# Kernel optimization log

Hardware: AMD Instinct MI355X
Metric: run time of the kernel (lower is better)

Reference implementation:

```python
import math
import jax, jax.numpy as jnp
import numpy as np

B, D, T, C, H = 4096, 1024, 768, 16, 4
CURV = 0.05
EPS = 1e-8
ASINH_MAX = float(np.arcsinh(2.0 ** 15))

# ---------- Poincare ball ops (hyptorch.pmath) ----------

def artanh(x):
    x = jnp.clip(x, -1 + 1e-5, 1 - 1e-5)
    return 0.5 * (jnp.log1p(x) - jnp.log1p(-x))

def p_logmap0(y, c):
    sc = c ** 0.5
    n = jnp.clip(jnp.linalg.norm(y, axis=-1, keepdims=True), 1e-15, None)
    return y / (n * sc) * artanh(sc * n)

def p_expmap0(u, c):
    sc = c ** 0.5
    n = jnp.clip(jnp.linalg.norm(u, axis=-1, keepdims=True), 1e-15, None)
    return jnp.tanh(sc * n) * u / (sc * n)

def p_project(x, c):
    maxn = (1 - 4e-3) / c ** 0.5  # float32 eps in hyptorch
    n = jnp.clip(jnp.linalg.norm(x, axis=-1, keepdims=True), 1e-15, None)
    return jnp.where(n > maxn, x / n * maxn, x)

# ---------- Lorentz ops (MERU-style L module) ----------

def l_expmap0(x, c):
    rc = (c ** 0.5) * jnp.linalg.norm(x, axis=-1, keepdims=True)
    si = jnp.clip(rc, EPS, ASINH_MAX)
    return jnp.sinh(si) * x / jnp.clip(rc, EPS, None)

def l_logmap0(x, c):
    rc = (c ** 0.5) * jnp.linalg.norm(x, axis=-1, keepdims=True)
    return jnp.arcsinh(rc) * x / jnp.clip(rc, EPS, None)

def oxy_angle(x, y, c):
    xt = jnp.sqrt(1.0 / c + jnp.sum(x * x, -1))
    yt = jnp.sqrt(1.0 / c + jnp.sum(y * y, -1))
    c_xyl = c * (jnp.sum(x * y, -1) - xt * yt)
    num = yt + c_xyl * xt
    den = jnp.sqrt(jnp.clip(c_xyl ** 2 - 1.0, EPS, None))
    acos_in = num / (jnp.linalg.norm(x, axis=-1) * den + EPS)
    return jnp.arccos(jnp.clip(acos_in, -1 + EPS, 1 - EPS))

def half_aperture(x, c, min_radius=0.1):
    asin_in = 2.0 * min_radius / (jnp.linalg.norm(x, axis=-1) * c ** 0.5 + EPS)
    return jnp.arcsin(jnp.clip(asin_in, -1 + EPS, 1 - EPS))

# ---------- small building blocks ----------

def layernorm(x, w, b, eps=1e-5):
    mu = jnp.mean(x, -1, keepdims=True)
    var = jnp.mean((x - mu) ** 2, -1, keepdims=True)
    return (x - mu) * jax.lax.rsqrt(var + eps) * w + b

def mha(x, w_in, b_in, w_out, b_out):
    # x: (B, S=4, D), torch nn.MultiheadAttention, batch_first, 4 heads
    Bq, S, Dm = x.shape
    hd = Dm // H
    qkv = x @ w_in.T + b_in
    q, k, v = jnp.split(qkv, 3, axis=-1)
    rs = lambda t: t.reshape(Bq, S, H, hd).transpose(0, 2, 1, 3)
    q, k, v = rs(q), rs(k), rs(v)
    a = jax.nn.softmax(jnp.einsum('bhqd,bhkd->bhqk', q, k) / math.sqrt(hd), axis=-1)
    o = jnp.einsum('bhqk,bhkd->bhqd', a, v).transpose(0, 2, 1, 3).reshape(Bq, S, Dm)
    return o @ w_out.T + b_out

def mobius_add_batch(x, y, c):
    # x: (C, D) (the -p points), y: (B, D) -> (C, B, D)
    xy = x @ y.T                               # (C, B)
    x2 = jnp.sum(x * x, -1, keepdims=True)     # (C, 1)
    y2 = jnp.sum(y * y, -1)                    # (B,)
    num = (1 + 2 * c * xy + c * y2[None, :])[..., None] * x[:, None, :] \
        + (1 - c * x2)[..., None] * y[None, :, :]
    den = 1 + 2 * c * xy + c * c * x2 * y2[None, :]
    return num / (den[..., None] + 1e-5)

def hyperbolic_mlr(x, a, p, c):
    sc = c ** 0.5
    p_p = p_expmap0(p, c)                      # (C, D)
    conf = 1 - c * jnp.sum(p_p ** 2, -1, keepdims=True)
    a_p = a * conf                             # (C, D)
    lam = 2.0 / (1 - c * jnp.sum(p_p ** 2, -1))
    a_norm = jnp.linalg.norm(a_p, axis=-1)     # (C,)
    kk = lam * a_norm / sc
    mob = mobius_add_batch(-p_p, x, c)         # (C, B, D)
    num = 2 * sc * jnp.einsum('cbd,cd->cb', mob, a_p)
    den = a_norm[:, None] * (1 - c * jnp.sum(mob ** 2, -1))
    return (kk[:, None] * jnp.arcsinh(num / den)).T  # (B, C)

def hyp_loss_fn(order_hyp, family_hyp, order, family, mask,
                to_w, to_b, tf_w, tf_b):
    order_feats = l_expmap0(order @ to_w.T + to_b, CURV)
    order_loss = jnp.mean(jax.nn.relu(
        oxy_angle(order_feats, family_hyp, CURV) - half_aperture(order_feats, CURV)))
    fam_feats = l_expmap0(family @ tf_w.T + tf_b, CURV)
    fpen = jax.nn.relu(
        oxy_angle(fam_feats, order_hyp, CURV) - half_aperture(fam_feats, CURV))
    m = mask.astype(order.dtype)
    cnt = jnp.sum(m)
    family_loss = jnp.where(cnt > 0, jnp.sum(fpen * m) / jnp.clip(cnt, 1.0, None), 0.0)
    return order_loss + family_loss


def setup_inputs() -> dict:
    key = jax.random.key(0)
    ks = jax.random.split(key, 20)
    g = lambda k, s, sc: jax.random.normal(k, s, jnp.float32) * sc
    inp = {
        # Poincare-ball points: scale down so sqrt(c)*||x|| << 1
        'order_hyp': g(ks[0], (B, D), 0.02),
        'family_hyp': g(ks[1], (B, D), 0.02),
        'order_euc': g(ks[2], (B, D), 1.0),
        'family_euc': g(ks[3], (B, D), 1.0),
        'order': g(ks[4], (B, T), 1.0),
        'family': g(ks[5], (B, T), 1.0),
        'mask': jax.random.randint(ks[6], (B,), 0, 2, jnp.int32),
        # MultiheadAttention params
        'in_proj_w': g(ks[7], (3 * D, D), D ** -0.5),
        'in_proj_b': jnp.zeros((3 * D,), jnp.float32),
        'out_proj_w': g(ks[8], (D, D), D ** -0.5),
        'out_proj_b': jnp.zeros((D,), jnp.float32),
        # LayerNorm
        'ln_w': jnp.ones((D,), jnp.float32),
        'ln_b': jnp.zeros((D,), jnp.float32),
        # text projections
        'to_w': g(ks[9], (D, T), T ** -0.5),
        'to_b': jnp.zeros((D,), jnp.float32),
        'tf_w': g(ks[10], (D, T), T ** -0.5),
        'tf_b': jnp.zeros((D,), jnp.float32),
        # HyperbolicMLR params
        'mlr_a': g(ks[11], (C, D), 0.02),
        'mlr_p': g(ks[12], (C, D), 0.02),
    }
    return inp


def reference(order_hyp, family_hyp, order_euc, family_euc, order, family, mask,
              in_proj_w, in_proj_b, out_proj_w, out_proj_b, ln_w, ln_b,
              to_w, to_b, tf_w, tf_b, mlr_a, mlr_p):
    # FromPoincare (logmap0 on the ball)
    fh_e = p_logmap0(family_hyp, CURV)
    oh_e = p_logmap0(order_hyp, CURV)
    gf = jnp.stack([oh_e, fh_e, order_euc, family_euc], axis=1)  # (B, 4, D)
    attn = mha(gf, in_proj_w, in_proj_b, out_proj_w, out_proj_b)
    gf = layernorm(gf + attn, ln_w, ln_b)
    oh, fh, oeu, feu = gf[:, 0], gf[:, 1], gf[:, 2], gf[:, 3]
    fh = l_expmap0(fh, CURV)
    oh = l_expmap0(oh, CURV)
    hyp_loss = hyp_loss_fn(oh, fh, order, family, mask, to_w, to_b, tf_w, tf_b)
    oh_out = l_logmap0(oh, CURV)
    hyp_pt = p_project(p_expmap0(oh_out, CURV), CURV)  # ToPoincare(riemannian=False)
    logits = hyperbolic_mlr(hyp_pt, mlr_a, mlr_p, CURV)
    return (logits, hyp_loss, oh, fh, oeu, feu)
```

## Files before the change

kernel.cpp:

```cpp
#include <hip/hip_runtime.h>
#include <stdint.h>

#define BB    4096
#define DD    1024
#define TT    768
#define CC    16
#define HH    4
#define SS    4
#define HD    256
#define M1    (BB*SS)
#define CURVF 0.05f
#define SCF   0.22360679774997896f
#define EPSF  1e-8f
#define ASINH_MAXF 11.090354888959125f

#define OFF_LOGITS 0ull
#define OFF_LOSS   65536ull
#define OFF_OH     65537ull
#define OFF_FH     (65537ull + 4194304ull)
#define OFF_OEU    (65537ull + 2ull*4194304ull)
#define OFF_FEU    (65537ull + 3ull*4194304ull)

typedef __attribute__((ext_vector_type(8))) short bf16x8;
typedef __attribute__((ext_vector_type(4))) float f32x4;

__device__ __forceinline__ float bf2f(unsigned short h) {
  union { unsigned int u; float f; } v; v.u = ((unsigned int)h) << 16; return v.f;
}
__device__ __forceinline__ unsigned short f2bf(float f) {
  union { float f; unsigned int u; } v; v.f = f;
  unsigned int u = v.u;
  return (unsigned short)((u + 0x7FFFu + ((u >> 16) & 1u)) >> 16);
}
__device__ __forceinline__ ushort4 f2bf4(float4 v) {
  ushort4 o; o.x = f2bf(v.x); o.y = f2bf(v.y); o.z = f2bf(v.z); o.w = f2bf(v.w);
  return o;
}
__device__ __forceinline__ float wsum(float v) {
#pragma unroll
  for (int o = 32; o > 0; o >>= 1) v += __shfl_xor(v, o, 64);
  return v;
}
__device__ __forceinline__ float block_sum(float v, float* red) {
  v = wsum(v);
  int lane = threadIdx.x & 63, wv = threadIdx.x >> 6;
  __syncthreads();
  if (lane == 0) red[wv] = v;
  __syncthreads();
  return red[0] + red[1] + red[2] + red[3];
}
__device__ __forceinline__ float artanh_clip(float x) {
  x = fminf(fmaxf(x, -1.0f + 1e-5f), 1.0f - 1e-5f);
  return 0.5f * (log1pf(x) - log1pf(-x));
}

typedef __attribute__((address_space(1))) const void gas_void;
typedef __attribute__((address_space(3))) void las_void;
__device__ __forceinline__ void gld16(void* l, const void* g) {
  __builtin_amdgcn_global_load_lds((gas_void*)g, (las_void*)l, 16, 0, 0);
}

#define VMCNT(n) asm volatile("s_waitcnt vmcnt(" #n ")" ::: "memory")

struct Cvt6 {
  const float4* src[6];
  unsigned short* dst[6];
  unsigned int end4[6];
};

__device__ __forceinline__ void prep_gf_body(const float* __restrict__ ohyp,
    const float* __restrict__ fhyp, const float* __restrict__ oeuc,
    const float* __restrict__ feuc, unsigned short* __restrict__ gf,
    int b, float* red) {
  int t = threadIdx.x;
  size_t base4 = (size_t)b * (DD / 4);
  float4 xo = ((const float4*)ohyp)[base4 + t];
  float4 xf = ((const float4*)fhyp)[base4 + t];
  float so = xo.x * xo.x + xo.y * xo.y + xo.z * xo.z + xo.w * xo.w;
  float sf = xf.x * xf.x + xf.y * xf.y + xf.z * xf.z + xf.w * xf.w;
  float no2 = block_sum(so, red);
  float nf2 = block_sum(sf, red);
  float no = fmaxf(sqrtf(no2), 1e-15f);
  float nf = fmaxf(sqrtf(nf2), 1e-15f);
  float fo = artanh_clip(SCF * no) / (no * SCF);
  float ff = artanh_clip(SCF * nf) / (nf * SCF);
  size_t g0 = (size_t)b * 4 * (DD / 4);
  float4 e2 = ((const float4*)oeuc)[base4 + t];
  float4 e3 = ((const float4*)feuc)[base4 + t];
  float4 y0 = {xo.x * fo, xo.y * fo, xo.z * fo, xo.w * fo};
  float4 y1 = {xf.x * ff, xf.y * ff, xf.z * ff, xf.w * ff};
  ((ushort4*)gf)[g0 + t]              = f2bf4(y0);
  ((ushort4*)gf)[g0 + DD / 4 + t]     = f2bf4(y1);
  ((ushort4*)gf)[g0 + 2 * DD / 4 + t] = f2bf4(e2);
  ((ushort4*)gf)[g0 + 3 * DD / 4 + t] = f2bf4(e3);
}

__device__ __forceinline__ void mlr_prep_body(const float* __restrict__ a,
    const float* __restrict__ p, float* __restrict__ p_p, float* __restrict__ a_p,
    float* __restrict__ cs, int c, float* red) {
  int t = threadIdx.x;
  size_t base4 = (size_t)c * (DD / 4);
  float4 pv = ((const float4*)p)[base4 + t];
  float4 av = ((const float4*)a)[base4 + t];
  float sp = pv.x * pv.x + pv.y * pv.y + pv.z * pv.z + pv.w * pv.w;
  float sa = av.x * av.x + av.y * av.y + av.z * av.z + av.w * av.w;
  float spa = pv.x * av.x + pv.y * av.y + pv.z * av.z + pv.w * av.w;
  sp = block_sum(sp, red); sa = block_sum(sa, red); spa = block_sum(spa, red);
  float n = fmaxf(sqrtf(sp), 1e-15f);
  float f = tanhf(SCF * n) / (SCF * n);
  float x2 = f * f * sp;
  float conf = 1.0f - CURVF * x2;
  float a_norm = fabsf(conf) * sqrtf(sa);
  float lam = 2.0f / (1.0f - CURVF * x2);
  float kk = lam * a_norm / SCF;
  float xa = -f * conf * spa;
  float4 pp = {pv.x * f, pv.y * f, pv.z * f, pv.w * f};
  float4 ap = {av.x * conf, av.y * conf, av.z * conf, av.w * conf};
  ((float4*)p_p)[base4 + t] = pp;
  ((float4*)a_p)[base4 + t] = ap;
  if (threadIdx.x == 0) {
    cs[c * 5 + 0] = x2; cs[c * 5 + 1] = conf; cs[c * 5 + 2] = a_norm;
    cs[c * 5 + 3] = kk; cs[c * 5 + 4] = xa;
  }
}

__global__ __launch_bounds__(256) void k_front(
    const float* __restrict__ ohyp, const float* __restrict__ fhyp,
    const float* __restrict__ oeuc, const float* __restrict__ feuc,
    unsigned short* __restrict__ gf,
    const float* __restrict__ mlr_a, const float* __restrict__ mlr_p,
    float* __restrict__ p_p, float* __restrict__ a_p, float* __restrict__ cs,
    Cvt6 cv, unsigned int total4) {
  __shared__ float red[4];
  unsigned int blk = blockIdx.x;
  if (blk < BB) {
    prep_gf_body(ohyp, fhyp, oeuc, feuc, gf, (int)blk, red);
    return;
  }
  if (blk < BB + CC) {
    mlr_prep_body(mlr_a, mlr_p, p_p, a_p, cs, (int)(blk - BB), red);
    return;
  }
  unsigned int i = (blk - BB - CC) * 256 + threadIdx.x;
  if (i >= total4) return;
#pragma unroll
  for (int j = 0; j < 6; j++) {
    if (i < cv.end4[j]) {
      unsigned int k = i - (j ? cv.end4[j - 1] : 0u);
      ((ushort4*)cv.dst[j])[k] = f2bf4(cv.src[j][k]);
      return;
    }
  }
}

template <int OUT_BF16>
__global__ __launch_bounds__(512) void k_gemm256(
    const unsigned short* __restrict__ A, const unsigned short* __restrict__ Bm,
    const float* __restrict__ bias, void* __restrict__ Cv,
    int N, int K, int nx) {
  __shared__ unsigned short lds[4][2][8192];
  const int nwg = gridDim.x;
  const int rid = blockIdx.x;
  const int wg = (rid & 7) * (nwg >> 3) + (rid >> 3);
  const int bx = wg % nx;
  const int by = wg / nx;
  const long tileM = (long)by * 256;
  const long tileN = (long)bx * 256;
  const int tid = threadIdx.x;
  const int lane = tid & 63;
  const int wv = tid >> 6;
  const int wr = wv >> 2;
  const int wc = wv & 3;
  const int NT = K >> 5;

  f32x4 acc[8][4];
#pragma unroll
  for (int i = 0; i < 8; i++)
#pragma unroll
    for (int j = 0; j < 4; j++) acc[i][j] = (f32x4){0.f, 0.f, 0.f, 0.f};

  const int srow = tid >> 2;
  const int lc = (tid & 3) ^ ((srow >> 1) & 3);
  const unsigned short* Ag = A + (tileM + srow) * (long)K + lc * 8;
  const unsigned short* Bg = Bm + (tileN + srow) * (long)K + lc * 8;

  auto stageA = [&](int t) {
    int b = t & 3;
    const unsigned short* s = Ag + t * 32;
    gld16(&lds[b][0][tid * 8], s);
    gld16(&lds[b][0][4096 + tid * 8], s + (long)128 * K);
  };
  auto stageB = [&](int t) {
    int b = t & 3;
    const unsigned short* s = Bg + t * 32;
    gld16(&lds[b][1][tid * 8], s);
    gld16(&lds[b][1][4096 + tid * 8], s + (long)128 * K);
  };

  stageA(0); stageB(0);
  stageA(1); stageB(1);
  stageA(2); stageB(2);
  VMCNT(8);
  __builtin_amdgcn_s_barrier();
  asm volatile("" ::: "memory");

  const int fr = lane & 15;
  const int hi = lane >> 4;
  const int fko = (hi ^ ((fr >> 1) & 3)) * 8;

  for (int t = 0; t < NT; ++t) {
    const unsigned short* Ab = &lds[t & 3][0][0];
    const unsigned short* Bb = &lds[t & 3][1][0];
    bf16x8 af[4], bfr[4];
#pragma unroll
    for (int j = 0; j < 4; j++)
      bfr[j] = *(const bf16x8*)(Bb + (wc * 64 + j * 16 + fr) * 32 + fko);
#pragma unroll
    for (int i = 0; i < 4; i++)
      af[i] = *(const bf16x8*)(Ab + (wr * 128 + i * 16 + fr) * 32 + fko);
    if (t + 3 < NT) stageA(t + 3);
    __builtin_amdgcn_s_setprio(1);
#pragma unroll
    for (int i = 0; i < 4; i++)
#pragma unroll
      for (int j = 0; j < 4; j++)
        acc[i][j] = __builtin_amdgcn_mfma_f32_16x16x32_bf16(af[i], bfr[j], acc[i][j], 0, 0, 0);
    __builtin_amdgcn_s_setprio(0);
#pragma unroll
    for (int i = 0; i < 4; i++)
      af[i] = *(const bf16x8*)(Ab + (wr * 128 + (i + 4) * 16 + fr) * 32 + fko);
    if (t + 3 < NT) stageB(t + 3);
    __builtin_amdgcn_s_setprio(1);
#pragma unroll
    for (int i = 0; i < 4; i++)
#pragma unroll
      for (int j = 0; j < 4; j++)
        acc[i + 4][j] = __builtin_amdgcn_mfma_f32_16x16x32_bf16(af[i], bfr[j], acc[i + 4][j], 0, 0, 0);
    __builtin_amdgcn_s_setprio(0);
    if (t + 1 < NT) {
      if (t + 3 < NT)      VMCNT(8);
      else if (t + 2 < NT) VMCNT(4);
      else                 VMCNT(0);
      __builtin_amdgcn_s_barrier();
      asm volatile("" ::: "memory");
    }
  }

  const int er = hi * 4;
#pragma unroll
  for (int i = 0; i < 8; i++) {
#pragma unroll
    for (int j = 0; j < 4; j++) {
      long col = tileN + wc * 64 + j * 16 + fr;
      float bv = bias ? bias[col] : 0.f;
#pragma unroll
      for (int r = 0; r < 4; r++) {
        long row = tileM + wr * 128 + i * 16 + er + r;
        float v = acc[i][j][r] + bv;
        if (OUT_BF16) ((unsigned short*)Cv)[row * (long)N + col] = f2bf(v);
        else          ((float*)Cv)[row * (long)N + col] = v;
      }
    }
  }
}

template <int OUT_BF16>
__device__ __forceinline__ void gemm_body(
    unsigned short* As, unsigned short* Bs,
    const unsigned short* __restrict__ A, const unsigned short* __restrict__ Bm,
    const float* __restrict__ bias, void* __restrict__ Cv,
    int M, int N, int K, int bx, int by) {
  const int tid = threadIdx.x;
  const int lane = tid & 63;
  const int wv = tid >> 6;
  const long tileM = (long)by * 128;
  const long tileN = (long)bx * 128;

  f32x4 acc[4][4];
#pragma unroll
  for (int i = 0; i < 4; i++)
#pragma unroll
    for (int j = 0; j < 4; j++) acc[i][j] = (f32x4){0.f, 0.f, 0.f, 0.f};

  const int srow = wv * 16 + (lane >> 2);
  const int lc = (lane & 3) ^ ((srow >> 1) & 3);
  const unsigned short* Ag = A + (tileM + srow) * (long)K + lc * 8;
  const unsigned short* Bg = Bm + (tileN + srow) * (long)K + lc * 8;
  unsigned short* Asl = As + srow * 32 + (lane & 3) * 8;
  unsigned short* Bsl = Bs + srow * 32 + (lane & 3) * 8;

  const int fr = lane & 15;
  const int rkey = (fr >> 1) & 3;
  const int fko2 = (((lane >> 4) ^ rkey)) * 8;
  const int wr = (wv >> 1) * 64;
  const int wc = (wv & 1) * 64;

  for (int k0 = 0; k0 < K; k0 += 32) {
    gld16(Asl, Ag + k0);
    gld16(Asl + 64 * 32, Ag + (long)64 * K + k0);
    gld16(Bsl, Bg + k0);
    gld16(Bsl + 64 * 32, Bg + (long)64 * K + k0);
    __syncthreads();
    bf16x8 af[4], bfr[4];
#pragma unroll
    for (int i = 0; i < 4; i++)
      af[i] = *(const bf16x8*)(As + (wr + i * 16 + fr) * 32 + fko2);
#pragma unroll
    for (int j = 0; j < 4; j++)
      bfr[j] = *(const bf16x8*)(Bs + (wc + j * 16 + fr) * 32 + fko2);
#pragma unroll
    for (int i = 0; i < 4; i++)
#pragma unroll
      for (int j = 0; j < 4; j++)
        acc[i][j] = __builtin_amdgcn_mfma_f32_16x16x32_bf16(af[i], bfr[j], acc[i][j], 0, 0, 0);
    __syncthreads();
  }

  const int er = (lane >> 4) * 4;
  const int ec = lane & 15;
#pragma unroll
  for (int i = 0; i < 4; i++) {
#pragma unroll
    for (int j = 0; j < 4; j++) {
      long col = tileN + wc + j * 16 + ec;
      float bv = bias ? bias[col] : 0.f;
#pragma unroll
      for (int r = 0; r < 4; r++) {
        long row = tileM + wr + i * 16 + er + r;
        float v = acc[i][j][r] + bv;
        if (OUT_BF16) ((unsigned short*)Cv)[row * (long)N + col] = f2bf(v);
        else          ((float*)Cv)[row * (long)N + col] = v;
      }
    }
  }
}

__global__ __launch_bounds__(256) void k_gemm_loss(
    const unsigned short* __restrict__ A0, const unsigned short* __restrict__ B0,
    const float* __restrict__ b0, float* __restrict__ C0,
    const unsigned short* __restrict__ A1, const unsigned short* __restrict__ B1,
    const float* __restrict__ b1, float* __restrict__ C1, int M, int N, int K) {
  __shared__ unsigned short As[128 * 32];
  __shared__ unsigned short Bs[128 * 32];
  if (blockIdx.z == 0)
    gemm_body<0>(As, Bs, A0, B0, b0, C0, M, N, K, blockIdx.x, blockIdx.y);
  else
    gemm_body<0>(As, Bs, A1, B1, b1, C1, M, N, K, blockIdx.x, blockIdx.y);
}

__global__ __launch_bounds__(256) void k_attn(const unsigned short* __restrict__ qkv,
                                              unsigned short* __restrict__ o) {
  int b = blockIdx.x;
  int h = blockIdx.y;
  int lane = threadIdx.x & 63;
  int qi = threadIdx.x >> 6;
  const unsigned short* base = qkv + (size_t)b * 4 * 3072 + h * HD;
  int d = lane * 4;
  float qv[4], kv[4][4], vv[4][4];
  {
    ushort4 q4 = *(const ushort4*)(base + (size_t)qi * 3072 + d);
    qv[0] = bf2f(q4.x); qv[1] = bf2f(q4.y); qv[2] = bf2f(q4.z); qv[3] = bf2f(q4.w);
  }
#pragma unroll
  for (int j = 0; j < 4; j++) {
    ushort4 k4 = *(const ushort4*)(base + (size_t)j * 3072 + 1024 + d);
    ushort4 v4 = *(const ushort4*)(base + (size_t)j * 3072 + 2048 + d);
    kv[j][0] = bf2f(k4.x); kv[j][1] = bf2f(k4.y); kv[j][2] = bf2f(k4.z); kv[j][3] = bf2f(k4.w);
    vv[j][0] = bf2f(v4.x); vv[j][1] = bf2f(v4.y); vv[j][2] = bf2f(v4.z); vv[j][3] = bf2f(v4.w);
  }
  float sc_[4];
#pragma unroll
  for (int j = 0; j < 4; j++) {
    float p = 0.f;
#pragma unroll
    for (int t = 0; t < 4; t++) p += qv[t] * kv[j][t];
    sc_[j] = wsum(p) * (1.0f / 16.0f);
  }
  float mx = fmaxf(fmaxf(sc_[0], sc_[1]), fmaxf(sc_[2], sc_[3]));
  float e[4], den = 0.f;
#pragma unroll
  for (int j = 0; j < 4; j++) { e[j] = expf(sc_[j] - mx); den += e[j]; }
  float inv = 1.0f / den;
  float4 ov = {0.f, 0.f, 0.f, 0.f};
#pragma unroll
  for (int j = 0; j < 4; j++) {
    float w = e[j] * inv;
    ov.x += w * vv[j][0]; ov.y += w * vv[j][1];
    ov.z += w * vv[j][2]; ov.w += w * vv[j][3];
  }
  *(ushort4*)(o + (size_t)(b * 4 + qi) * DD + h * HD + d) = f2bf4(ov);
}

__global__ __launch_bounds__(256) void k_ln_split(const unsigned short* __restrict__ gf,
    const unsigned short* __restrict__ attn, const float* __restrict__ lnw,
    const float* __restrict__ lnb, float* __restrict__ dout) {
  __shared__ float red[4];
  int r = blockIdx.x;
  int b = r >> 2, s = r & 3;
  int t = threadIdx.x;
  size_t base4 = (size_t)r * (DD / 4);
  ushort4 g4 = ((const ushort4*)gf)[base4 + t];
  ushort4 a4 = ((const ushort4*)attn)[base4 + t];
  float x[4] = {bf2f(g4.x) + bf2f(a4.x), bf2f(g4.y) + bf2f(a4.y),
                bf2f(g4.z) + bf2f(a4.z), bf2f(g4.w) + bf2f(a4.w)};
  float sum = x[0] + x[1] + x[2] + x[3];
  float sq = x[0] * x[0] + x[1] * x[1] + x[2] * x[2] + x[3] * x[3];
  sum = block_sum(sum, red);
  sq  = block_sum(sq, red);
  float mu = sum * (1.0f / (float)DD);
  float var = sq * (1.0f / (float)DD) - mu * mu;
  float inv = rsqrtf(var + 1e-5f);
  float4 w4 = ((const float4*)lnw)[t];
  float4 b4 = ((const float4*)lnb)[t];
  float y[4];
  y[0] = (x[0] - mu) * inv * w4.x + b4.x;
  y[1] = (x[1] - mu) * inv * w4.y + b4.y;
  y[2] = (x[2] - mu) * inv * w4.z + b4.z;
  y[3] = (x[3] - mu) * inv * w4.w + b4.w;
  float fmul = 1.0f;
  if (s < 2) {
    float n2 = y[0] * y[0] + y[1] * y[1] + y[2] * y[2] + y[3] * y[3];
    n2 = block_sum(n2, red);
    float rc = SCF * sqrtf(n2);
    float si = fminf(fmaxf(rc, EPSF), ASINH_MAXF);
    fmul = sinhf(si) / fmaxf(rc, EPSF);
  }
  size_t offs = (s == 0) ? OFF_OH : (s == 1) ? OFF_FH : (s == 2) ? OFF_OEU : OFF_FEU;
  float4* outp = (float4*)(dout + offs + (size_t)b * DD);
  float4 o4 = {y[0] * fmul, y[1] * fmul, y[2] * fmul, y[3] * fmul};
  outp[t] = o4;
}

__global__ __launch_bounds__(256) void k_oxy(const float* __restrict__ raw0,
    const float* __restrict__ y0, const float* __restrict__ raw1,
    const float* __restrict__ y1, float* __restrict__ pens) {
  __shared__ float red[4];
  int b = blockIdx.x;
  int which = blockIdx.y;
  const float* raw = which ? raw1 : raw0;
  const float* yr  = which ? y1 : y0;
  size_t base = (size_t)b * DD;
  float sxx = 0.f, sxy = 0.f, syy = 0.f;
#pragma unroll
  for (int k = 0; k < 4; k++) {
    int d = threadIdx.x + 256 * k;
    float xv = raw[base + d];
    float yv = yr[base + d];
    sxx += xv * xv; sxy += xv * yv; syy += yv * yv;
  }
  sxx = block_sum(sxx, red);
  sxy = block_sum(sxy, red);
  syy = block_sum(syy, red);
  if (threadIdx.x == 0) {
    float nraw = sqrtf(sxx);
    float rc = SCF * nraw;
    float si = fminf(fmaxf(rc, EPSF), ASINH_MAXF);
    float f = sinhf(si) / fmaxf(rc, EPSF);
    float x2 = f * f * sxx;
    float xy = f * sxy;
    float y2 = syy;
    float nx = f * nraw;
    float xt = sqrtf(1.0f / CURVF + x2);
    float yt = sqrtf(1.0f / CURVF + y2);
    float c_xyl = CURVF * (xy - xt * yt);
    float num = yt + c_xyl * xt;
    float den = sqrtf(fmaxf(c_xyl * c_xyl - 1.0f, EPSF));
    float ai = num / (nx * den + EPSF);
    ai = fminf(fmaxf(ai, -1.0f + EPSF), 1.0f - EPSF);
    float ang = acosf(ai);
    float asi = 0.2f / (nx * SCF + EPSF);
    asi = fminf(fmaxf(asi, -1.0f + EPSF), 1.0f - EPSF);
    float ap = asinf(asi);
    pens[(size_t)which * BB + b] = fmaxf(ang - ap, 0.0f);
  }
}

__global__ __launch_bounds__(256) void k_back(const float* __restrict__ oh,
    const float* __restrict__ p_p, const float* __restrict__ a_p,
    const float* __restrict__ cs, float* __restrict__ logits,
    const float* __restrict__ pens, const int* __restrict__ mask,
    float* __restrict__ dout) {
  __shared__ float row[DD];
  __shared__ float dots[CC][2];
  __shared__ float s_n2;
  __shared__ float red[4];
  int blk = blockIdx.x;
  int lane = threadIdx.x & 63, wv = threadIdx.x >> 6;

  if (blk == BB) {
    float s0 = 0.f, s1 = 0.f, cnt = 0.f;
    for (int i = threadIdx.x; i < BB; i += 256) {
      s0 += pens[i];
      float m = (float)mask[i];
      s1 += pens[BB + i] * m;
      cnt += m;
    }
    s0 = block_sum(s0, red);
    s1 = block_sum(s1, red);
    cnt = block_sum(cnt, red);
    if (threadIdx.x == 0) {
      float order_loss = s0 / (float)BB;
      float fam = (cnt > 0.f) ? s1 / fmaxf(cnt, 1.0f) : 0.0f;
      dout[OFF_LOSS] = order_loss + fam;
    }
    return;
  }

  int b = blk;
  const float* src = oh + (size_t)b * DD;
#pragma unroll
  for (int k = 0; k < 4; k++)
    row[threadIdx.x + 256 * k] = src[threadIdx.x + 256 * k];
  __syncthreads();
  if (wv == 0) {
    float n2p = 0.f;
#pragma unroll
    for (int k = 0; k < 4; k++) {
      float4 v = ((const float4*)row)[lane + 64 * k];
      n2p += v.x * v.x + v.y * v.y + v.z * v.z + v.w * v.w;
    }
    n2p = wsum(n2p);
    if (lane == 0) s_n2 = n2p;
  }
#pragma unroll
  for (int ccc = 0; ccc < 4; ccc++) {
    int c = wv * 4 + ccc;
    const float4* pp4 = (const float4*)(p_p + (size_t)c * DD);
    const float4* ap4 = (const float4*)(a_p + (size_t)c * DD);
    float dp = 0.f, da = 0.f;
#pragma unroll
    for (int k = 0; k < 4; k++) {
      int d4 = lane + 64 * k;
      float4 v = ((const float4*)row)[d4];
      float4 p4 = pp4[d4];
      float4 a4 = ap4[d4];
      dp += p4.x * v.x + p4.y * v.y + p4.z * v.z + p4.w * v.w;
      da += a4.x * v.x + a4.y * v.y + a4.z * v.z + a4.w * v.w;
    }
    dp = wsum(dp); da = wsum(da);
    if (lane == 0) { dots[c][0] = dp; dots[c][1] = da; }
  }
  __syncthreads();
  if (threadIdx.x < CC) {
    int c = threadIdx.x;
    float n2 = s_n2;
    float n1 = sqrtf(n2);
    float rc = SCF * n1;
    float g = asinhf(rc) / fmaxf(rc, EPSF);
    float nu = fmaxf(n1 * g, 1e-15f);
    float fac = tanhf(SCF * nu) / (SCF * nu);
    float s = g * fac;
    float ny = fmaxf(n1 * s, 1e-15f);
    float maxn = (1.0f - 0.004f) / SCF;
    if (ny > maxn) s *= maxn / ny;
    float y2 = s * s * n2;
    float py = s * dots[c][0];
    float ay = s * dots[c][1];
    float x2 = cs[c * 5 + 0], conf = cs[c * 5 + 1], a_norm = cs[c * 5 + 2];
    float kk = cs[c * 5 + 3], xa = cs[c * 5 + 4];
    float xy = -py;
    float A = 1.f + 2.f * CURVF * xy + CURVF * y2;
    float den0 = 1.f + 2.f * CURVF * xy + CURVF * CURVF * x2 * y2;
    float d = den0 + 1e-5f;
    float num = 2.f * SCF * (A * xa + conf * ay) / d;
    float mob2 = (A * A * x2 + 2.f * A * conf * xy + conf * conf * y2) / (d * d);
    float denl = a_norm * (1.f - CURVF * mob2);
    logits[(size_t)b * CC + c] = kk * asinhf(num / denl);
  }
}

extern "C" void kernel_launch(void* const* d_in, const int* in_sizes, int n_in,
                              void* d_out, int out_size, void* d_ws, size_t ws_size,
                              hipStream_t stream) {
  const float* order_hyp  = (const float*)d_in[0];
  const float* family_hyp = (const float*)d_in[1];
  const float* order_euc  = (const float*)d_in[2];
  const float* family_euc = (const float*)d_in[3];
  const float* order      = (const float*)d_in[4];
  const float* family     = (const float*)d_in[5];
  const int*   mask       = (const int*)d_in[6];
  const float* in_proj_w  = (const float*)d_in[7];
  const float* in_proj_b  = (const float*)d_in[8];
  const float* out_proj_w = (const float*)d_in[9];
  const float* out_proj_b = (const float*)d_in[10];
  const float* ln_w       = (const float*)d_in[11];
  const float* ln_b       = (const float*)d_in[12];
  const float* to_w       = (const float*)d_in[13];
  const float* to_b       = (const float*)d_in[14];
  const float* tf_w       = (const float*)d_in[15];
  const float* tf_b       = (const float*)d_in[16];
  const float* mlr_a      = (const float*)d_in[17];
  const float* mlr_p      = (const float*)d_in[18];
  float* dout = (float*)d_out;

  char* w = (char*)d_ws;
  size_t off = 0;
  auto take = [&](size_t n) { char* p = w + off; off += (n + 255) & ~(size_t)255; return p; };
  unsigned short* gf_bf   = (unsigned short*)take((size_t)M1 * DD * 2);
  unsigned short* region2 = (unsigned short*)take((size_t)M1 * 3 * DD * 2);
  unsigned short* o_bf    = (unsigned short*)take((size_t)M1 * DD * 2);
  unsigned short* win_bf  = (unsigned short*)take((size_t)3 * DD * DD * 2);
  unsigned short* wout_bf = (unsigned short*)take((size_t)DD * DD * 2);
  unsigned short* tow_bf  = (unsigned short*)take((size_t)DD * TT * 2);
  unsigned short* tfw_bf  = (unsigned short*)take((size_t)DD * TT * 2);
  unsigned short* ord_bf  = (unsigned short*)take((size_t)BB * TT * 2);
  unsigned short* fam_bf  = (unsigned short*)take((size_t)BB * TT * 2);
  float* p_p   = (float*)take((size_t)CC * DD * 4);
  float* a_p   = (float*)take((size_t)CC * DD * 4);
  float* cs    = (float*)take(CC * 5 * 4);
  float* pens  = (float*)take((size_t)2 * BB * 4);

  unsigned short* qkv     = region2;
  unsigned short* attn_bf = region2;
  float* ofeat = (float*)((char*)region2 + 33554432);
  float* ffeat = (float*)((char*)region2 + 50331648);

  Cvt6 cv;
  cv.src[0] = (const float4*)in_proj_w;  cv.dst[0] = win_bf;
  cv.src[1] = (const float4*)out_proj_w; cv.dst[1] = wout_bf;
  cv.src[2] = (const float4*)to_w;       cv.dst[2] = tow_bf;
  cv.src[3] = (const float4*)tf_w;       cv.dst[3] = tfw_bf;
  cv.src[4] = (const float4*)order;      cv.dst[4] = ord_bf;
  cv.src[5] = (const float4*)family;     cv.dst[5] = fam_bf;
  unsigned int n4[6] = {3u * DD * DD / 4, DD * DD / 4, DD * TT / 4, DD * TT / 4,
                        BB * TT / 4, BB * TT / 4};
  unsigned int acc4 = 0;
  for (int j = 0; j < 6; j++) { acc4 += n4[j]; cv.end4[j] = acc4; }
  unsigned int cvtBlocks = (acc4 + 255) / 256;
  k_front<<<BB + CC + cvtBlocks, 256, 0, stream>>>(
      order_hyp, family_hyp, order_euc, family_euc, gf_bf,
      mlr_a, mlr_p, p_p, a_p, cs, cv, acc4);

  {
    int nx = 3 * DD / 256, ny = M1 / 256;
    k_gemm256<1><<<nx * ny, 512, 0, stream>>>(
        gf_bf, win_bf, in_proj_b, qkv, 3 * DD, DD, nx);
  }

  k_attn<<<dim3(BB, HH), 256, 0, stream>>>(qkv, o_bf);

  {
    int nx = DD / 256, ny = M1 / 256;
    k_gemm256<1><<<nx * ny, 512, 0, stream>>>(
        o_bf, wout_bf, out_proj_b, attn_bf, DD, DD, nx);
  }

  k_ln_split<<<M1, 256, 0, stream>>>(gf_bf, attn_bf, ln_w, ln_b, dout);

  k_gemm_loss<<<dim3(DD / 128, BB / 128, 2), 256, 0, stream>>>(
      ord_bf, tow_bf, to_b, ofeat, fam_bf, tfw_bf, tf_b, ffeat, BB, DD, TT);

  k_oxy<<<dim3(BB, 2), 256, 0, stream>>>(ofeat, dout + OFF_FH, ffeat, dout + OFF_OH, pens);

  k_back<<<BB + 1, 256, 0, stream>>>(dout + OFF_OH, p_p, a_p, cs,
                                     dout + OFF_LOGITS, pens, mask, dout);

  (void)in_sizes; (void)n_in; (void)out_size; (void)ws_size;
}
```

Baseline: 456.4 us.

## Merge loss-feature GEMMs into QKV GEMM launch and fuse oxy into layernorm

The two loss-feature GEMMs (order/family projections) are now computed with the tuned 256x256 pipelined GEMM body inside the same launch as the QKV projection, replacing the older 128-tile kernel. The separate oxy-angle kernel is folded into the layernorm/split kernel, which reuses the freshly normalised and expmapped values already in registers instead of re-reading them. The feature buffers move to dedicated workspace because they must now live across the attention and output-projection stages, which costs extra workspace memory. Two launches are removed and the small GEMMs get a more efficient kernel and fill tail waves of the big one.

New measurement: 445.1 us. -2.5%, faster.

```diff
diff --git a/kernel.cpp b/kernel.cpp
--- a/kernel.cpp
+++ b/kernel.cpp
@@ -153,17 +153,11 @@
   }
 }
 
-template <int OUT_BF16>
-__global__ __launch_bounds__(512) void k_gemm256(
+__device__ __forceinline__ void gemm256_body(
     const unsigned short* __restrict__ A, const unsigned short* __restrict__ Bm,
     const float* __restrict__ bias, void* __restrict__ Cv,
-    int N, int K, int nx) {
-  __shared__ unsigned short lds[4][2][8192];
-  const int nwg = gridDim.x;
-  const int rid = blockIdx.x;
-  const int wg = (rid & 7) * (nwg >> 3) + (rid >> 3);
-  const int bx = wg % nx;
-  const int by = wg / nx;
+    int N, int K, int bx, int by, int out_bf16,
+    unsigned short (*lds)[2][8192]) {
   const long tileM = (long)by * 256;
   const long tileN = (long)bx * 256;
   const int tid = threadIdx.x;
@@ -247,105 +241,69 @@
   }
 
   const int er = hi * 4;
-#pragma unroll
-  for (int i = 0; i < 8; i++) {
-#pragma unroll
-    for (int j = 0; j < 4; j++) {
-      long col = tileN + wc * 64 + j * 16 + fr;
-      float bv = bias ? bias[col] : 0.f;
-#pragma unroll
-      for (int r = 0; r < 4; r++) {
-        long row = tileM + wr * 128 + i * 16 + er + r;
-        float v = acc[i][j][r] + bv;
-        if (OUT_BF16) ((unsigned short*)Cv)[row * (long)N + col] = f2bf(v);
-        else          ((float*)Cv)[row * (long)N + col] = v;
+  if (out_bf16) {
+#pragma unroll
+    for (int i = 0; i < 8; i++)
+#pragma unroll
+      for (int j = 0; j < 4; j++) {
+        long col = tileN + wc * 64 + j * 16 + fr;
+        float bv = bias ? bias[col] : 0.f;
+#pragma unroll
+        for (int r = 0; r < 4; r++) {
+          long row = tileM + wr * 128 + i * 16 + er + r;
+          ((unsigned short*)Cv)[row * (long)N + col] = f2bf(acc[i][j][r] + bv);
+        }
       }
-    }
+  } else {
+#pragma unroll
+    for (int i = 0; i < 8; i++)
+#pragma unroll
+      for (int j = 0; j < 4; j++) {
+        long col = tileN + wc * 64 + j * 16 + fr;
+        float bv = bias ? bias[col] : 0.f;
+#pragma unroll
+        for (int r = 0; r < 4; r++) {
+          long row = tileM + wr * 128 + i * 16 + er + r;
+          ((float*)Cv)[row * (long)N + col] = acc[i][j][r] + bv;
+        }
+      }
   }
 }
 
 template <int OUT_BF16>
-__device__ __forceinline__ void gemm_body(
-    unsigned short* As, unsigned short* Bs,
+__global__ __launch_bounds__(512) void k_gemm256(
     const unsigned short* __restrict__ A, const unsigned short* __restrict__ Bm,
     const float* __restrict__ bias, void* __restrict__ Cv,
-    int M, int N, int K, int bx, int by) {
-  const int tid = threadIdx.x;
-  const int lane = tid & 63;
-  const int wv = tid >> 6;
-  const long tileM = (long)by * 128;
-  const long tileN = (long)bx * 128;
-
-  f32x4 acc[4][4];
-#pragma unroll
-  for (int i = 0; i < 4; i++)
-#pragma unroll
-    for (int j = 0; j < 4; j++) acc[i][j] = (f32x4){0.f, 0.f, 0.f, 0.f};
-
-  const int srow = wv * 16 + (lane >> 2);
-  const int lc = (lane & 3) ^ ((srow >> 1) & 3);
-  const unsigned short* Ag = A + (tileM + srow) * (long)K + lc * 8;
-  const unsigned short* Bg = Bm + (tileN + srow) * (long)K + lc * 8;
-  unsigned short* Asl = As + srow * 32 + (lane & 3) * 8;
-  unsigned short* Bsl = Bs + srow * 32 + (lane & 3) * 8;
-
-  const int fr = lane & 15;
-  const int rkey = (fr >> 1) & 3;
-  const int fko2 = (((lane >> 4) ^ rkey)) * 8;
-  const int wr = (wv >> 1) * 64;
-  const int wc = (wv & 1) * 64;
-
-  for (int k0 = 0; k0 < K; k0 += 32) {
-    gld16(Asl, Ag + k0);
-    gld16(Asl + 64 * 32, Ag + (long)64 * K + k0);
-    gld16(Bsl, Bg + k0);
-    gld16(Bsl + 64 * 32, Bg + (long)64 * K + k0);
-    __syncthreads();
-    bf16x8 af[4], bfr[4];
-#pragma unroll
-    for (int i = 0; i < 4; i++)
-      af[i] = *(const bf16x8*)(As + (wr + i * 16 + fr) * 32 + fko2);
-#pragma unroll
-    for (int j = 0; j < 4; j++)
-      bfr[j] = *(const bf16x8*)(Bs + (wc + j * 16 + fr) * 32 + fko2);
-#pragma unroll
-    for (int i = 0; i < 4; i++)
-#pragma unroll
-      for (int j = 0; j < 4; j++)
-        acc[i][j] = __builtin_amdgcn_mfma_f32_16x16x32_bf16(af[i], bfr[j], acc[i][j], 0, 0, 0);
-    __syncthreads();
-  }
-
-  const int er = (lane >> 4) * 4;
-  const int ec = lane & 15;
-#pragma unroll
-  for (int i = 0; i < 4; i++) {
-#pragma unroll
-    for (int j = 0; j < 4; j++) {
-      long col = tileN + wc + j * 16 + ec;
-      float bv = bias ? bias[col] : 0.f;
-#pragma unroll
-      for (int r = 0; r < 4; r++) {
-        long row = tileM + wr + i * 16 + er + r;
-        float v = acc[i][j][r] + bv;
-        if (OUT_BF16) ((unsigned short*)Cv)[row * (long)N + col] = f2bf(v);
-        else          ((float*)Cv)[row * (long)N + col] = v;
-      }
-    }
-  }
-}
-
-__global__ __launch_bounds__(256) void k_gemm_loss(
+    int N, int K, int nx) {
+  __shared__ unsigned short lds[4][2][8192];
+  const int nwg = gridDim.x;
+  const int rid = blockIdx.x;
+  const int wg = (rid & 7) * (nwg >> 3) + (rid >> 3);
+  gemm256_body(A, Bm, bias, Cv, N, K, wg % nx, wg / nx, OUT_BF16, lds);
+}
+
+__global__ __launch_bounds__(512) void k_gemm_merged(
     const unsigned short* __restrict__ A0, const unsigned short* __restrict__ B0,
-    const float* __restrict__ b0, float* __restrict__ C0,
+    const float* __restrict__ bias0, void* __restrict__ C0, int N0, int K0,
+    int nx0, int nwg0,
     const unsigned short* __restrict__ A1, const unsigned short* __restrict__ B1,
-    const float* __restrict__ b1, float* __restrict__ C1, int M, int N, int K) {
-  __shared__ unsigned short As[128 * 32];
-  __shared__ unsigned short Bs[128 * 32];
-  if (blockIdx.z == 0)
-    gemm_body<0>(As, Bs, A0, B0, b0, C0, M, N, K, blockIdx.x, blockIdx.y);
-  else
-    gemm_body<0>(As, Bs, A1, B1, b1, C1, M, N, K, blockIdx.x, blockIdx.y);
+    const float* __restrict__ bias1, void* __restrict__ C1,
+    const unsigned short* __restrict__ A2, const unsigned short* __restrict__ B2,
+    const float* __restrict__ bias2, void* __restrict__ C2,
+    int N12, int K12, int nx12, int nwg1) {
+  __shared__ unsigned short lds[4][2][8192];
+  const int nwg = gridDim.x;
+  const int rid = blockIdx.x;
+  const int wg = (rid & 7) * (nwg >> 3) + (rid >> 3);
+  if (wg < nwg0) {
+    gemm256_body(A0, B0, bias0, C0, N0, K0, wg % nx0, wg / nx0, 1, lds);
+  } else if (wg < nwg0 + nwg1) {
+    int w = wg - nwg0;
+    gemm256_body(A1, B1, bias1, C1, N12, K12, w % nx12, w / nx12, 0, lds);
+  } else {
+    int w = wg - nwg0 - nwg1;
+    gemm256_body(A2, B2, bias2, C2, N12, K12, w % nx12, w / nx12, 0, lds);
+  }
 }
 
 __global__ __launch_bounds__(256) void k_attn(const unsigned short* __restrict__ qkv,
@@ -391,9 +349,11 @@
   *(ushort4*)(o + (size_t)(b * 4 + qi) * DD + h * HD + d) = f2bf4(ov);
 }
 
-__global__ __launch_bounds__(256) void k_ln_split(const unsigned short* __restrict__ gf,
+__global__ __launch_bounds__(256) void k_ln_oxy(const unsigned short* __restrict__ gf,
     const unsigned short* __restrict__ attn, const float* __restrict__ lnw,
-    const float* __restrict__ lnb, float* __restrict__ dout) {
+    const float* __restrict__ lnb, const float* __restrict__ ofeat,
+    const float* __restrict__ ffeat, float* __restrict__ pens,
+    float* __restrict__ dout) {
   __shared__ float red[4];
   int r = blockIdx.x;
   int b = r >> 2, s = r & 3;
@@ -429,49 +389,39 @@
   float4* outp = (float4*)(dout + offs + (size_t)b * DD);
   float4 o4 = {y[0] * fmul, y[1] * fmul, y[2] * fmul, y[3] * fmul};
   outp[t] = o4;
-}
-
-__global__ __launch_bounds__(256) void k_oxy(const float* __restrict__ raw0,
-    const float* __restrict__ y0, const float* __restrict__ raw1,
-    const float* __restrict__ y1, float* __restrict__ pens) {
-  __shared__ float red[4];
-  int b = blockIdx.x;
-  int which = blockIdx.y;
-  const float* raw = which ? raw1 : raw0;
-  const float* yr  = which ? y1 : y0;
-  size_t base = (size_t)b * DD;
-  float sxx = 0.f, sxy = 0.f, syy = 0.f;
-#pragma unroll
-  for (int k = 0; k < 4; k++) {
-    int d = threadIdx.x + 256 * k;
-    float xv = raw[base + d];
-    float yv = yr[base + d];
-    sxx += xv * xv; sxy += xv * yv; syy += yv * yv;
-  }
-  sxx = block_sum(sxx, red);
-  sxy = block_sum(sxy, red);
-  syy = block_sum(syy, red);
-  if (threadIdx.x == 0) {
-    float nraw = sqrtf(sxx);
-    float rc = SCF * nraw;
-    float si = fminf(fmaxf(rc, EPSF), ASINH_MAXF);
-    float f = sinhf(si) / fmaxf(rc, EPSF);
-    float x2 = f * f * sxx;
-    float xy = f * sxy;
-    float y2 = syy;
-    float nx = f * nraw;
-    float xt = sqrtf(1.0f / CURVF + x2);
-    float yt = sqrtf(1.0f / CURVF + y2);
-    float c_xyl = CURVF * (xy - xt * yt);
-    float num = yt + c_xyl * xt;
-    float den = sqrtf(fmaxf(c_xyl * c_xyl - 1.0f, EPSF));
-    float ai = num / (nx * den + EPSF);
-    ai = fminf(fmaxf(ai, -1.0f + EPSF), 1.0f - EPSF);
-    float ang = acosf(ai);
-    float asi = 0.2f / (nx * SCF + EPSF);
-    asi = fminf(fmaxf(asi, -1.0f + EPSF), 1.0f - EPSF);
-    float ap = asinf(asi);
-    pens[(size_t)which * BB + b] = fmaxf(ang - ap, 0.0f);
+
+  if (s < 2) {
+    const float* raw = (s == 0) ? ffeat : ofeat;
+    float4 rv = ((const float4*)(raw + (size_t)b * DD))[t];
+    float sxx = rv.x * rv.x + rv.y * rv.y + rv.z * rv.z + rv.w * rv.w;
+    float sxy = rv.x * o4.x + rv.y * o4.y + rv.z * o4.z + rv.w * o4.w;
+    float syy = o4.x * o4.x + o4.y * o4.y + o4.z * o4.z + o4.w * o4.w;
+    sxx = block_sum(sxx, red);
+    sxy = block_sum(sxy, red);
+    syy = block_sum(syy, red);
+    if (t == 0) {
+      float nraw = sqrtf(sxx);
+      float rc2 = SCF * nraw;
+      float si2 = fminf(fmaxf(rc2, EPSF), ASINH_MAXF);
+      float f = sinhf(si2) / fmaxf(rc2, EPSF);
+      float x2 = f * f * sxx;
+      float xy = f * sxy;
+      float y2 = syy;
+      float nx = f * nraw;
+      float xt = sqrtf(1.0f / CURVF + x2);
+      float yt = sqrtf(1.0f / CURVF + y2);
+      float c_xyl = CURVF * (xy - xt * yt);
+      float num = yt + c_xyl * xt;
+      float den = sqrtf(fmaxf(c_xyl * c_xyl - 1.0f, EPSF));
+      float ai = num / (nx * den + EPSF);
+      ai = fminf(fmaxf(ai, -1.0f + EPSF), 1.0f - EPSF);
+      float ang = acosf(ai);
+      float asi = 0.2f / (nx * SCF + EPSF);
+      asi = fminf(fmaxf(asi, -1.0f + EPSF), 1.0f - EPSF);
+      float ap = asinf(asi);
+      int which = (s == 0) ? 1 : 0;
+      pens[(size_t)which * BB + b] = fmaxf(ang - ap, 0.0f);
+    }
   }
 }
 
@@ -609,11 +559,11 @@
   float* a_p   = (float*)take((size_t)CC * DD * 4);
   float* cs    = (float*)take(CC * 5 * 4);
   float* pens  = (float*)take((size_t)2 * BB * 4);
+  float* ofeat = (float*)take((size_t)BB * DD * 4);
+  float* ffeat = (float*)take((size_t)BB * DD * 4);
 
   unsigned short* qkv     = region2;
   unsigned short* attn_bf = region2;
-  float* ofeat = (float*)((char*)region2 + 33554432);
-  float* ffeat = (float*)((char*)region2 + 50331648);
 
   Cvt6 cv;
   cv.src[0] = (const float4*)in_proj_w;  cv.dst[0] = win_bf;
@@ -632,9 +582,16 @@
       mlr_a, mlr_p, p_p, a_p, cs, cv, acc4);
 
   {
-    int nx = 3 * DD / 256, ny = M1 / 256;
-    k_gemm256<1><<<nx * ny, 512, 0, stream>>>(
-        gf_bf, win_bf, in_proj_b, qkv, 3 * DD, DD, nx);
+    int nx0 = 3 * DD / 256, ny0 = M1 / 256;
+    int nwg0 = nx0 * ny0;
+    int nx12 = DD / 256, ny12 = BB / 256;
+    int nwg1 = nx12 * ny12;
+    int total = nwg0 + 2 * nwg1;
+    k_gemm_merged<<<total, 512, 0, stream>>>(
+        gf_bf, win_bf, in_proj_b, qkv, 3 * DD, DD, nx0, nwg0,
+        ord_bf, tow_bf, to_b, ofeat,
+        fam_bf, tfw_bf, tf_b, ffeat,
+        DD, TT, nx12, nwg1);
   }
 
   k_attn<<<dim3(BB, HH), 256, 0, stream>>>(qkv, o_bf);
@@ -645,12 +602,8 @@
         o_bf, wout_bf, out_proj_b, attn_bf, DD, DD, nx);
   }
 
-  k_ln_split<<<M1, 256, 0, stream>>>(gf_bf, attn_bf, ln_w, ln_b, dout);
-
-  k_gemm_loss<<<dim3(DD / 128, BB / 128, 2), 256, 0, stream>>>(
-      ord_bf, tow_bf, to_b, ofeat, fam_bf, tfw_bf, tf_b, ffeat, BB, DD, TT);
-
-  k_oxy<<<dim3(BB, 2), 256, 0, stream>>>(ofeat, dout + OFF_FH, ffeat, dout + OFF_OH, pens);
+  k_ln_oxy<<<M1, 256, 0, stream>>>(gf_bf, attn_bf, ln_w, ln_b,
+                                   ofeat, ffeat, pens, dout);
 
   k_back<<<BB + 1, 256, 0, stream>>>(dout + OFF_OH, p_p, a_p, cs,
                                      dout + OFF_LOGITS, pens, mask, dout);
```
